# Kernel optimization log

Hardware: AMD Instinct MI355X
Metric: run time of the kernel (lower is better)

The kernel has to match this reference:

```python
import jax, jax.numpy as jnp
import numpy as np

N = 50000   # nodes
E = 200000  # edges per relation
R = 4       # relations
IN = 128
HID = 32
H = 4
OUT = 32


def setup_inputs() -> dict:
    key = jax.random.key(0)
    ks = jax.random.split(key, 32)
    w = lambda k, shape: jax.random.normal(k, shape, jnp.float32) * 0.05
    inp = {
        "x": jax.random.normal(ks[0], (N, IN), jnp.float32),
        "edge_src": jax.random.randint(ks[1], (R, E), 0, N, dtype=jnp.int32),
        "edge_dst": jax.random.randint(ks[2], (R, E), 0, N, dtype=jnp.int32),
    }
    # (d_in, heads*d_out, d_out) per layer: flatten, flatten, mean-over-heads
    dims = [(IN, H * HID, HID), (H * HID, H * HID, HID), (H * HID, H * OUT, OUT)]
    i = 3
    for l, (din, dout, d) in enumerate(dims):
        inp[f"Wsrc{l}"] = w(ks[i], (R, din, dout)); i += 1
        inp[f"bsrc{l}"] = w(ks[i], (R, dout)); i += 1
        inp[f"Wdst{l}"] = w(ks[i], (R, din, dout)); i += 1
        inp[f"bdst{l}"] = w(ks[i], (R, dout)); i += 1
        inp[f"attn{l}"] = w(ks[i], (R, H, d)); i += 1
    return inp


def rel_gatv2(h, src, dst, Ws, bs, Wd, bd, att):
    """DGL GATv2Conv for one relation: gather, leaky-relu score, edge softmax, scatter-sum."""
    n = h.shape[0]
    heads, d = att.shape
    fs = (h @ Ws + bs).reshape(n, heads, d)   # [N,H,D]
    fd = (h @ Wd + bd).reshape(n, heads, d)
    e = jax.nn.leaky_relu(fs[src] + fd[dst], 0.2)        # [E,H,D]
    score = jnp.einsum('ehd,hd->eh', e, att)             # [E,H]
    # numerically stable edge softmax segmented by destination node
    m = jax.lax.stop_gradient(jax.ops.segment_max(score, dst, num_segments=n))
    m = jnp.where(jnp.isfinite(m), m, 0.0)               # zero-in-degree guard
    ex = jnp.exp(score - m[dst])
    den = jax.ops.segment_sum(ex, dst, num_segments=n)
    a = ex / jnp.maximum(den[dst], 1e-16)                # [E,H]
    return jax.ops.segment_sum(a[:, :, None] * fs[src], dst, num_segments=n)  # [N,H,D]


def gat_layer(h, edge_src, edge_dst, Ws, bs, Wd, bd, att, mean_heads):
    out = None
    for r in range(Ws.shape[0]):  # small fixed relation count; HeteroGraphConv sums
        o = rel_gatv2(h, edge_src[r], edge_dst[r], Ws[r], bs[r], Wd[r], bd[r], att[r])
        out = o if out is None else out + o
    if mean_heads:                # last_layer_flag: mean over heads
        return out.mean(axis=1)
    return out.reshape(h.shape[0], -1)  # flatten heads


def reference(x, edge_src, edge_dst,
              Wsrc0, bsrc0, Wdst0, bdst0, attn0,
              Wsrc1, bsrc1, Wdst1, bdst1, attn1,
              Wsrc2, bsrc2, Wdst2, bdst2, attn2):
    h = gat_layer(x, edge_src, edge_dst, Wsrc0, bsrc0, Wdst0, bdst0, attn0, False)
    h = gat_layer(h, edge_src, edge_dst, Wsrc1, bsrc1, Wdst1, bdst1, attn1, False)
    h = gat_layer(h, edge_src, edge_dst, Wsrc2, bsrc2, Wdst2, bdst2, attn2, True)
    return h  # [N, OUT]
```

## Files before the change

kernel.cpp:

```cpp
#include <hip/hip_runtime.h>
#include <math.h>

#define FF 128
#define CAP 32
#define GB 512

typedef _Float16 half2v __attribute__((ext_vector_type(2)));
typedef _Float16 f16x8  __attribute__((ext_vector_type(8)));
typedef __fp16   fp16x2 __attribute__((ext_vector_type(2)));
typedef __attribute__((ext_vector_type(4))) float f4v;

__device__ __forceinline__ half2v u2h(unsigned u) {
    union { unsigned u; half2v h; } c; c.u = u; return c.h;
}
__device__ __forceinline__ unsigned h2u(half2v h) {
    union { unsigned u; half2v h; } c; c.h = h; return c.u;
}
__device__ __forceinline__ unsigned short f2h(float f) {
    _Float16 h = (_Float16)f;
    unsigned short u; __builtin_memcpy(&u, &h, 2); return u;
}
__device__ __forceinline__ half2v pk2h(float e) {
    union { fp16x2 p; half2v h; } c;
    c.p = __builtin_amdgcn_cvt_pkrtz(e, e);
    return c.h;
}
__device__ __forceinline__ float dot2(half2v a, half2v b, float c) {
#if __has_builtin(__builtin_amdgcn_fdot2)
    union { half2v h; fp16x2 p; } ca, cb;
    ca.h = a; cb.h = b;
    return __builtin_amdgcn_fdot2(ca.p, cb.p, c, false);
#else
    return c + (float)a.x * (float)b.x + (float)a.y * (float)b.y;
#endif
}

__global__ __launch_bounds__(256, 2) void setup_fused(
    const float* __restrict__ x,
    const float* __restrict__ W0s_, const float* __restrict__ bs0,
    const float* __restrict__ W0d_, const float* __restrict__ bd0,
    unsigned short* __restrict__ fs_all, unsigned short* __restrict__ fd_all,
    int nrb, int n,
    const int* __restrict__ esrc_all, const int* __restrict__ edst_all,
    int* __restrict__ cursor, int* __restrict__ slots, int totalE, int ne,
    const float* __restrict__ W1s_, const float* __restrict__ W1d_,
    const float* __restrict__ W2s_, const float* __restrict__ W2d_,
    unsigned short* __restrict__ Wp,
    const float* __restrict__ a0, const float* __restrict__ a1,
    const float* __restrict__ a2, unsigned* __restrict__ attH,
    int CB)
{
    int b = blockIdx.x;
    const int tid = threadIdx.x;

    if (b < GB) {
        const int wave = tid >> 6, lane = tid & 63;
        const int r = b & 3;
        const int half = wave & 1;
        const int lo = lane & 15, quad = lane >> 4;

        unsigned short* fs = fs_all + (size_t)r * n * FF;
        unsigned short* fd = fd_all + (size_t)r * n * FF;

        f16x8 B[2][4][4];
        #pragma unroll
        for (int mat = 0; mat < 2; ++mat) {
            const float* W = (mat == 0) ? W0s_ : W0d_;
            #pragma unroll
            for (int nbi = 0; nbi < 4; ++nbi)
                #pragma unroll
                for (int ks = 0; ks < 4; ++ks) {
                    const int nn = (half * 4 + nbi) * 16 + lo;
                    f16x8 v;
                    #pragma unroll
                    for (int j = 0; j < 8; ++j) {
                        const int k = ks * 32 + quad * 8 + j;
                        v[j] = (_Float16)W[((size_t)r * FF + k) * FF + nn];
                    }
                    B[mat][nbi][ks] = v;
                }
        }

        float biasS[4], biasD[4];
        #pragma unroll
        for (int nbi = 0; nbi < 4; ++nbi) {
            biasS[nbi] = bs0[r * FF + (half * 4 + nbi) * 16 + lo];
            biasD[nbi] = bd0[r * FF + (half * 4 + nbi) * 16 + lo];
        }

        const int stride = (GB >> 2) * 2;
        for (int rb = (b >> 2) * 2 + (wave >> 1); rb < nrb; rb += stride) {
            const int row0 = rb * 16;
            f16x8 A[4];
            #pragma unroll
            for (int ks = 0; ks < 4; ++ks) {
                const float* ap = &x[(size_t)(row0 + lo) * FF + ks * 32 + quad * 8];
                const float4 p0 = *(const float4*)&ap[0];
                const float4 p1 = *(const float4*)&ap[4];
                f16x8 v;
                v[0] = (_Float16)p0.x; v[1] = (_Float16)p0.y;
                v[2] = (_Float16)p0.z; v[3] = (_Float16)p0.w;
                v[4] = (_Float16)p1.x; v[5] = (_Float16)p1.y;
                v[6] = (_Float16)p1.z; v[7] = (_Float16)p1.w;
                A[ks] = v;
            }

            f4v cS[4], cD[4];
            #pragma unroll
            for (int nbi = 0; nbi < 4; ++nbi) {
                cS[nbi] = (f4v){biasS[nbi], biasS[nbi], biasS[nbi], biasS[nbi]};
                cD[nbi] = (f4v){biasD[nbi], biasD[nbi], biasD[nbi], biasD[nbi]};
            }

            #pragma unroll
            for (int ks = 0; ks < 4; ++ks)
                #pragma unroll
                for (int nbi = 0; nbi < 4; ++nbi) {
                    cS[nbi] = __builtin_amdgcn_mfma_f32_16x16x32_f16(
                        A[ks], B[0][nbi][ks], cS[nbi], 0, 0, 0);
                    cD[nbi] = __builtin_amdgcn_mfma_f32_16x16x32_f16(
                        A[ks], B[1][nbi][ks], cD[nbi], 0, 0, 0);
                }

            #pragma unroll
            for (int nbi = 0; nbi < 4; ++nbi)
                #pragma unroll
                for (int i = 0; i < 4; ++i) {
                    const size_t o = (size_t)(row0 + quad * 4 + i) * FF
                                   + (half * 4 + nbi) * 16 + lo;
                    fs[o] = f2h(cS[nbi][i]);
                    fd[o] = f2h(cD[nbi][i]);
                }
        }
        return;
    }
    b -= GB;

    if (b < CB) {
        const int t0 = b * 1024 + tid;
        #pragma unroll
        for (int k = 0; k < 4; ++k) {
            const int i = t0 + k * 256;
            if (i < totalE) {
                const int r = i / ne;
                const int rd = r * 50000 + edst_all[i];
                const int idx = atomicAdd(&cursor[rd], 1);
                slots[(size_t)rd * CAP + idx] = esrc_all[i];
            }
        }
        return;
    }
    b -= CB;

    if (b < 1536) {
        const int t = b * 256 + tid;
        if (t >= 3 * 4 * 2 * FF * FF) return;
        const int l    = t >> 17;
        const int rest = t & 131071;
        const int r    = rest >> 15;
        const int mat  = (rest >> 14) & 1;
        const int idx  = rest & 16383;
        const int k = idx >> 7, nn = idx & 127;
        const float* W = (l == 0) ? (mat ? W0d_ : W0s_)
                       : (l == 1) ? (mat ? W1d_ : W1s_)
                                  : (mat ? W2d_ : W2s_);
        const float v = W[((size_t)r * FF + k) * FF + nn];
        const int nb = nn >> 4, lo = nn & 15;
        const int ks = k >> 5, quad = (k >> 3) & 3, j = k & 7;
        const int lane = quad * 16 + lo;
        const size_t o = (((((((size_t)l * 4 + r) * 2 + mat) * 8 + nb) * 4 + ks) * 64 + lane) * 8) + j;
        Wp[o] = f2h(v);
        return;
    }
    b -= 1536;

    const int t = b * 256 + tid;
    if (t >= 768) return;
    const int l = t >> 8, rest = t & 255;
    const float* a = (l == 0) ? a0 : (l == 1) ? a1 : a2;
    const float2 v = ((const float2*)a)[rest];
    half2v h = {(_Float16)v.x, (_Float16)v.y};
    attH[t] = h2u(h);
}

__global__ __launch_bounds__(256, 2) void mfma_gemm(
    const unsigned short* __restrict__ hb,
    const unsigned short* __restrict__ Wp,
    const float* __restrict__ bs_all,
    const float* __restrict__ bd_all,
    unsigned short* __restrict__ fs_all,
    unsigned short* __restrict__ fd_all,
    int nrb, int n)
{
    const int wave = threadIdx.x >> 6, lane = threadIdx.x & 63;
    const int r = blockIdx.x & 3;
    const int half = wave & 1;
    const int lo = lane & 15, quad = lane >> 4;

    const unsigned short* Wr = Wp + (size_t)r * 2 * FF * FF;
    unsigned short* fs = fs_all + (size_t)r * n * FF;
    unsigned short* fd = fd_all + (size_t)r * n * FF;

    f16x8 B[2][4][4];
    #pragma unroll
    for (int mat = 0; mat < 2; ++mat)
        #pragma unroll
        for (int nbi = 0; nbi < 4; ++nbi)
            #pragma unroll
            for (int ks = 0; ks < 4; ++ks) {
                const int nb = half * 4 + nbi;
                B[mat][nbi][ks] = *(const f16x8*)
                    &Wr[(((((size_t)mat * 8 + nb) * 4 + ks) * 64 + lane) * 8)];
            }

    float biasS[4], biasD[4];
    #pragma unroll
    for (int nbi = 0; nbi < 4; ++nbi) {
        biasS[nbi] = bs_all[r * FF + (half * 4 + nbi) * 16 + lo];
        biasD[nbi] = bd_all[r * FF + (half * 4 + nbi) * 16 + lo];
    }

    const int stride = (gridDim.x >> 2) * 2;
    for (int rb = (blockIdx.x >> 2) * 2 + (wave >> 1); rb < nrb; rb += stride) {
        const int row0 = rb * 16;
        f16x8 A[4];
        #pragma unroll
        for (int ks = 0; ks < 4; ++ks)
            A[ks] = *(const f16x8*)&hb[(size_t)(row0 + lo) * FF + ks * 32 + quad * 8];

        f4v cS[4], cD[4];
        #pragma unroll
        for (int nbi = 0; nbi < 4; ++nbi) {
            cS[nbi] = (f4v){biasS[nbi], biasS[nbi], biasS[nbi], biasS[nbi]};
            cD[nbi] = (f4v){biasD[nbi], biasD[nbi], biasD[nbi], biasD[nbi]};
        }

        #pragma unroll
        for (int ks = 0; ks < 4; ++ks)
            #pragma unroll
            for (int nbi = 0; nbi < 4; ++nbi) {
                cS[nbi] = __builtin_amdgcn_mfma_f32_16x16x32_f16(
                    A[ks], B[0][nbi][ks], cS[nbi], 0, 0, 0);
                cD[nbi] = __builtin_amdgcn_mfma_f32_16x16x32_f16(
                    A[ks], B[1][nbi][ks], cD[nbi], 0, 0, 0);
            }

        #pragma unroll
        for (int nbi = 0; nbi < 4; ++nbi)
            #pragma unroll
            for (int i = 0; i < 4; ++i) {
                const size_t o = (size_t)(row0 + quad * 4 + i) * FF
                               + (half * 4 + nbi) * 16 + lo;
                fs[o] = f2h(cS[nbi][i]);
                fd[o] = f2h(cD[nbi][i]);
            }
    }
}

__device__ __forceinline__ void edge4(
    uint4 g, bool ok, const half2v* fdv, const half2v* atv,
    float& den, half2v* acc)
{
    const half2v C02 = {(_Float16)0.2f, (_Float16)0.2f};
    half2v f[4] = {u2h(g.x), u2h(g.y), u2h(g.z), u2h(g.w)};
    float v = 0.f;
    #pragma unroll
    for (int i = 0; i < 4; ++i) {
        const half2v z = f[i] + fdv[i];
        const half2v l = __builtin_elementwise_max(z, z * C02);
        v = dot2(l, atv[i], v);
    }
    v += __shfl_xor(v, 2);
    v += __shfl_xor(v, 1);
    const float e = ok ? __expf(v) : 0.f;
    den += e;
    const half2v eh = pk2h(e);
    #pragma unroll
    for (int i = 0; i < 4; ++i) acc[i] += eh * f[i];
}

__global__ __launch_bounds__(256) void aggregate(
    const int* __restrict__ cnt,
    const int* __restrict__ slots,
    const unsigned* __restrict__ fs_all,
    const unsigned* __restrict__ fd_all,
    const unsigned* __restrict__ att_h,
    unsigned* __restrict__ out_h,
    float* __restrict__ out_f32,
    int n)
{
    const int node = blockIdx.x * 4 + (threadIdx.x >> 6);
    if (node >= n) return;
    const int lane = threadIdx.x & 63;
    const int quarter = lane >> 4;
    const int q = lane & 15;
    const int fo = 4 * q;

    int m[4]; int4 sA[4];
    #pragma unroll
    for (int r = 0; r < 4; ++r) {
        const size_t rd = (size_t)r * n + node;
        m[r]  = cnt[rd];
        sA[r] = *(const int4*)&slots[rd * CAP];
    }

    float val[8] = {0.f, 0.f, 0.f, 0.f, 0.f, 0.f, 0.f, 0.f};

    #pragma unroll
    for (int r = 0; r < 4; ++r) {
        const int mr = m[r];
        if (mr == 0) continue;
        const size_t rd = (size_t)r * n + node;
        const unsigned* fsu = fs_all + (size_t)r * n * 64;

        const int4 sB = *(const int4*)&slots[rd * CAP + 4];
        const uint4 ufd = *(const uint4*)&fd_all[rd * 64 + fo];
        const uint4 uat = *(const uint4*)&att_h[r * 64 + fo];
        half2v fdv[4] = {u2h(ufd.x), u2h(ufd.y), u2h(ufd.z), u2h(ufd.w)};
        half2v atv[4] = {u2h(uat.x), u2h(uat.y), u2h(uat.z), u2h(uat.w)};

        const bool ok0 = quarter < mr;
        const bool ok1 = 4 + quarter < mr;
        int i0 = (quarter == 0) ? sA[r].x : (quarter == 1) ? sA[r].y
               : (quarter == 2) ? sA[r].z : sA[r].w;
        int i1 = (quarter == 0) ? sB.x : (quarter == 1) ? sB.y
               : (quarter == 2) ? sB.z : sB.w;
        i0 = ok0 ? i0 : 0;
        i1 = ok1 ? i1 : 0;
        const uint4 g0 = *(const uint4*)&fsu[(size_t)i0 * 64 + fo];
        const uint4 g1 = *(const uint4*)&fsu[(size_t)i1 * 64 + fo];

        float den = 0.f;
        half2v acc[4];
        #pragma unroll
        for (int i = 0; i < 4; ++i) acc[i] = (half2v){(_Float16)0.f, (_Float16)0.f};

        edge4(g0, ok0, fdv, atv, den, acc);
        if (mr > 4)
            edge4(g1, ok1, fdv, atv, den, acc);

        if (mr > 8) {
            const int* sl = slots + rd * CAP;
            for (int p = 8; p < mr; p += 4) {
                const int ei = p + quarter;
                const bool ok = ei < mr;
                int s = sl[ei < CAP ? ei : CAP - 1]; s = ok ? s : 0;
                const uint4 g = *(const uint4*)&fsu[(size_t)s * 64 + fo];
                edge4(g, ok, fdv, atv, den, acc);
            }
        }

        den += __shfl_xor(den, 16);
        den += __shfl_xor(den, 32);
        const float inv = (den > 0.f) ? 1.f / den : 0.f;
        #pragma unroll
        for (int i = 0; i < 4; ++i) {
            val[2 * i]     += (float)acc[i].x * inv;
            val[2 * i + 1] += (float)acc[i].y * inv;
        }
    }

    #pragma unroll
    for (int i = 0; i < 8; ++i) {
        val[i] += __shfl_xor(val[i], 16);
        val[i] += __shfl_xor(val[i], 32);
    }

    if (out_f32) {
        #pragma unroll
        for (int i = 0; i < 8; ++i) {
            val[i] += __shfl_xor(val[i], 4);
            val[i] += __shfl_xor(val[i], 8);
        }
        if (lane < 4) {
            float* o = &out_f32[(size_t)node * 32 + 8 * lane];
            *(float4*)&o[0] = make_float4(0.25f * val[0], 0.25f * val[1],
                                          0.25f * val[2], 0.25f * val[3]);
            *(float4*)&o[4] = make_float4(0.25f * val[4], 0.25f * val[5],
                                          0.25f * val[6], 0.25f * val[7]);
        }
    } else {
        if (lane < 16) {
            uint4 o;
            o.x = h2u((half2v){(_Float16)val[0], (_Float16)val[1]});
            o.y = h2u((half2v){(_Float16)val[2], (_Float16)val[3]});
            o.z = h2u((half2v){(_Float16)val[4], (_Float16)val[5]});
            o.w = h2u((half2v){(_Float16)val[6], (_Float16)val[7]});
            *(uint4*)&out_h[(size_t)node * 64 + fo] = o;
        }
    }
}

extern "C" void kernel_launch(void* const* d_in, const int* in_sizes, int n_in,
                              void* d_out, int out_size, void* d_ws, size_t ws_size,
                              hipStream_t stream)
{
    const int n  = in_sizes[0] / FF;
    const int R  = 4;
    const int ne = in_sizes[1] / R;
    const int totalE = R * ne;
    const int L  = R * n;
    const int nrb = (n + 15) / 16;

    const float* x    = (const float*)d_in[0];
    const int*   esrc = (const int*)d_in[1];
    const int*   edst = (const int*)d_in[2];

    char* p = (char*)d_ws;
    auto carve = [&p](size_t bytes) { char* q = p; p += (bytes + 255) & ~(size_t)255; return q; };
    unsigned*       hbA    = (unsigned*)      carve((size_t)n * 64 * 4);
    unsigned*       hbB    = (unsigned*)      carve((size_t)n * 64 * 4);
    unsigned short* fs_all = (unsigned short*)carve((size_t)R * n * FF * 2);
    unsigned short* fd_all = (unsigned short*)carve((size_t)R * n * FF * 2);
    unsigned short* Wp     = (unsigned short*)carve((size_t)3 * R * 2 * FF * FF * 2);
    unsigned*       attH   = (unsigned*)      carve((size_t)3 * R * 64 * 4);
    int*            cursor = (int*)           carve((size_t)L * 4);
    int*            slots  = (int*)           carve((size_t)L * CAP * 4);

    (void)hipMemsetAsync(cursor, 0, (size_t)L * sizeof(int), stream);

    const int CB = (totalE + 1023) / 1024;
    setup_fused<<<GB + CB + 1536 + 3, 256, 0, stream>>>(
        x,
        (const float*)d_in[3], (const float*)d_in[4],
        (const float*)d_in[5], (const float*)d_in[6],
        fs_all, fd_all, nrb, n,
        esrc, edst, cursor, slots, totalE, ne,
        (const float*)d_in[8],  (const float*)d_in[10],
        (const float*)d_in[13], (const float*)d_in[15],
        Wp,
        (const float*)d_in[7], (const float*)d_in[12], (const float*)d_in[17],
        attH, CB);

    unsigned* bufs[3] = {hbA, hbB, nullptr};
    for (int l = 0; l < 3; ++l) {
        if (l > 0) {
            const float* bsrc = (const float*)d_in[3 + 5 * l + 1];
            const float* bdst = (const float*)d_in[3 + 5 * l + 3];
            mfma_gemm<<<512, 256, 0, stream>>>(
                (const unsigned short*)bufs[l - 1],
                Wp + (size_t)l * R * 2 * FF * FF,
                bsrc, bdst, fs_all, fd_all, nrb, n);
        }
        const int last = (l == 2);
        aggregate<<<(n + 3) / 4, 256, 0, stream>>>(
            cursor, slots,
            (const unsigned*)fs_all, (const unsigned*)fd_all,
            attH + (size_t)l * R * 64,
            last ? nullptr : bufs[l],
            last ? (float*)d_out : nullptr, n);
    }
}
```

Before: 420.9 us.

## Interleave GEMM and CSR blocks in setup; accumulate aggregation output in fp16

The fused setup kernel's block scheduling is changed so the layer-0 GEMM blocks and CSR-building blocks alternate in the first 2*GB block IDs. The aim is to overlap compute-bound MFMA work with atomic-heavy scatter work on the same CUs. The aggregation kernel now keeps per-node accumulators in packed fp16, scales by an approximate reciprocal, and does its cross-lane reductions with packed-half shuffles. This cuts conversions and shuffle count at the cost of precision. It also drops the zero-denominator guard, which risks inf/NaN for nodes with zero in-degree. The layout assumes CB >= GB.

```diff
diff --git a/kernel.cpp b/kernel.cpp
--- a/kernel.cpp
+++ b/kernel.cpp
@@ -33,6 +33,9 @@
 #else
     return c + (float)a.x * (float)b.x + (float)a.y * (float)b.y;
 #endif
+}
+__device__ __forceinline__ half2v shfladd_h(half2v v, int mask) {
+    return v + u2h(__shfl_xor(h2u(v), mask));
 }
 
 __global__ __launch_bounds__(256, 2) void setup_fused(
@@ -50,10 +53,23 @@
     const float* __restrict__ a2, unsigned* __restrict__ attH,
     int CB)
 {
-    int b = blockIdx.x;
     const int tid = threadIdx.x;
-
-    if (b < GB) {
+    int role, b;
+    if (blockIdx.x < 2 * GB) {
+        role = blockIdx.x & 1;
+        b = blockIdx.x >> 1;
+    } else {
+        int rest = blockIdx.x - 2 * GB;
+        const int csrRest = CB - GB;
+        if (rest < csrRest) { role = 1; b = GB + rest; }
+        else {
+            rest -= csrRest;
+            if (rest < 1536) { role = 2; b = rest; }
+            else             { role = 3; b = rest - 1536; }
+        }
+    }
+
+    if (role == 0) {
         const int wave = tid >> 6, lane = tid & 63;
         const int r = b & 3;
         const int half = wave & 1;
@@ -134,25 +150,23 @@
         }
         return;
     }
-    b -= GB;
-
-    if (b < CB) {
+
+    if (role == 1) {
         const int t0 = b * 1024 + tid;
         #pragma unroll
         for (int k = 0; k < 4; ++k) {
             const int i = t0 + k * 256;
             if (i < totalE) {
                 const int r = i / ne;
-                const int rd = r * 50000 + edst_all[i];
+                const int rd = r * n + edst_all[i];
                 const int idx = atomicAdd(&cursor[rd], 1);
                 slots[(size_t)rd * CAP + idx] = esrc_all[i];
             }
         }
         return;
     }
-    b -= CB;
-
-    if (b < 1536) {
+
+    if (role == 2) {
         const int t = b * 256 + tid;
         if (t >= 3 * 4 * 2 * FF * FF) return;
         const int l    = t >> 17;
@@ -172,7 +186,6 @@
         Wp[o] = f2h(v);
         return;
     }
-    b -= 1536;
 
     const int t = b * 256 + tid;
     if (t >= 768) return;
@@ -304,7 +317,9 @@
         sA[r] = *(const int4*)&slots[rd * CAP];
     }
 
-    float val[8] = {0.f, 0.f, 0.f, 0.f, 0.f, 0.f, 0.f, 0.f};
+    half2v val[4];
+    #pragma unroll
+    for (int i = 0; i < 4; ++i) val[i] = (half2v){(_Float16)0.f, (_Float16)0.f};
 
     #pragma unroll
     for (int r = 0; r < 4; ++r) {
@@ -352,40 +367,35 @@
 
         den += __shfl_xor(den, 16);
         den += __shfl_xor(den, 32);
-        const float inv = (den > 0.f) ? 1.f / den : 0.f;
+        const half2v ih = pk2h(__builtin_amdgcn_rcpf(den));
+        #pragma unroll
+        for (int i = 0; i < 4; ++i) val[i] += acc[i] * ih;
+    }
+
+    #pragma unroll
+    for (int i = 0; i < 4; ++i) {
+        val[i] = shfladd_h(val[i], 16);
+        val[i] = shfladd_h(val[i], 32);
+    }
+
+    if (out_f32) {
         #pragma unroll
         for (int i = 0; i < 4; ++i) {
-            val[2 * i]     += (float)acc[i].x * inv;
-            val[2 * i + 1] += (float)acc[i].y * inv;
-        }
-    }
-
-    #pragma unroll
-    for (int i = 0; i < 8; ++i) {
-        val[i] += __shfl_xor(val[i], 16);
-        val[i] += __shfl_xor(val[i], 32);
-    }
-
-    if (out_f32) {
-        #pragma unroll
-        for (int i = 0; i < 8; ++i) {
-            val[i] += __shfl_xor(val[i], 4);
-            val[i] += __shfl_xor(val[i], 8);
+            val[i] = shfladd_h(val[i], 4);
+            val[i] = shfladd_h(val[i], 8);
         }
         if (lane < 4) {
             float* o = &out_f32[(size_t)node * 32 + 8 * lane];
-            *(float4*)&o[0] = make_float4(0.25f * val[0], 0.25f * val[1],
-                                          0.25f * val[2], 0.25f * val[3]);
-            *(float4*)&o[4] = make_float4(0.25f * val[4], 0.25f * val[5],
-                                          0.25f * val[6], 0.25f * val[7]);
+            *(float4*)&o[0] = make_float4(0.25f * (float)val[0].x, 0.25f * (float)val[0].y,
+                                          0.25f * (float)val[1].x, 0.25f * (float)val[1].y);
+            *(float4*)&o[4] = make_float4(0.25f * (float)val[2].x, 0.25f * (float)val[2].y,
+                                          0.25f * (float)val[3].x, 0.25f * (float)val[3].y);
         }
     } else {
         if (lane < 16) {
             uint4 o;
-            o.x = h2u((half2v){(_Float16)val[0], (_Float16)val[1]});
-            o.y = h2u((half2v){(_Float16)val[2], (_Float16)val[3]});
-            o.z = h2u((half2v){(_Float16)val[4], (_Float16)val[5]});
-            o.w = h2u((half2v){(_Float16)val[6], (_Float16)val[7]});
+            o.x = h2u(val[0]); o.y = h2u(val[1]);
+            o.z = h2u(val[2]); o.w = h2u(val[3]);
             *(uint4*)&out_h[(size_t)node * 64 + fo] = o;
         }
     }
@@ -420,7 +430,7 @@
     (void)hipMemsetAsync(cursor, 0, (size_t)L * sizeof(int), stream);
 
     const int CB = (totalE + 1023) / 1024;
-    setup_fused<<<GB + CB + 1536 + 3, 256, 0, stream>>>(
+    setup_fused<<<2 * GB + (CB - GB) + 1536 + 3, 256, 0, stream>>>(
         x,
         (const float*)d_in[3], (const float*)d_in[4],
         (const float*)d_in[5], (const float*)d_in[6],
```

New measurement: 432.0 us. 1.03x slower.
